# Kernel optimization log

Measured on AMD Instinct MI355X. Metric: run time of the kernel, lower is better.

The kernel has to match this reference:

```python
import jax, jax.numpy as jnp
import numpy as np

N, K, B, D, T = 30000, 32, 8, 256, 10
NC = T + 1            # int_small_classes
LB_COL, UB_COL = 21, 22
INF = 1e18


def _ln(x, g, b, eps=1e-5):
    m = jnp.mean(x, axis=-1, keepdims=True)
    v = jnp.mean((x - m) ** 2, axis=-1, keepdims=True)
    return (x - m) * jax.lax.rsqrt(v + eps) * g + b


def _head(x, ng, nb, W1, b1, W2, b2, Wh, bh):
    # LayerNorm -> Linear -> GELU -> Linear -> GELU -> residual -> head (dropout off: eval)
    h = _ln(x, ng, nb)
    h = jax.nn.gelu(h @ W1.T + b1, approximate=False)
    h = jax.nn.gelu(h @ W2.T + b2, approximate=False)
    return (x + h) @ Wh.T + bh


def setup_inputs():
    key = jax.random.key(0)
    ks = jax.random.split(key, 32)
    s = 0.05
    inp = {}
    inp['evolved_tokens'] = jax.random.normal(ks[0], (B * K, D), jnp.float32)
    inp['var_batch'] = jnp.sort(jax.random.randint(ks[1], (N,), 0, B))
    aw = jax.random.uniform(ks[2], (N, K), jnp.float32)
    inp['attn_weights'] = aw / aw.sum(-1, keepdims=True)
    inp['var_types'] = jax.random.randint(ks[3], (N,), 0, 3)
    inp['z_var_0'] = jax.random.normal(ks[4], (N, D), jnp.float32)
    vf = 0.1 * jax.random.normal(ks[5], (N, 23), jnp.float32)
    lb = jnp.floor(jax.random.uniform(ks[6], (N,), minval=-5.0, maxval=0.0))
    ub = lb + jnp.floor(jax.random.uniform(ks[7], (N,), minval=0.0, maxval=30.0))
    ub = jnp.where(jax.random.uniform(ks[8], (N,)) < 0.1, 1e19, ub)
    inp['variable_features'] = vf.at[:, LB_COL].set(lb).at[:, UB_COL].set(ub)
    # deslice proj + fusion norm
    inp['Wp'] = s * jax.random.normal(ks[9], (D, D), jnp.float32)
    inp['bp'] = jnp.zeros((D,), jnp.float32)
    inp['fn_g'] = jnp.ones((D,), jnp.float32)
    inp['fn_b'] = jnp.zeros((D,), jnp.float32)
    # three decoder heads
    i = 10
    for name, out in (('bin', 1), ('ints', NC), ('intl', 1)):
        inp[name + '_ng'] = jnp.ones((D,), jnp.float32)
        inp[name + '_nb'] = jnp.zeros((D,), jnp.float32)
        inp[name + '_W1'] = s * jax.random.normal(ks[i], (D, D), jnp.float32)
        inp[name + '_b1'] = jnp.zeros((D,), jnp.float32)
        inp[name + '_W2'] = s * jax.random.normal(ks[i + 1], (D, D), jnp.float32)
        inp[name + '_b2'] = jnp.zeros((D,), jnp.float32)
        inp[name + '_Wh'] = s * jax.random.normal(ks[i + 2], (out, D), jnp.float32)
        inp[name + '_bh'] = (jnp.full((out,), -0.5, jnp.float32) if name == 'bin'
                             else jnp.zeros((out,), jnp.float32))
        i += 3
    return inp


def reference(evolved_tokens, var_batch, attn_weights, var_types, z_var_0,
              variable_features, Wp, bp, fn_g, fn_b,
              bin_ng, bin_nb, bin_W1, bin_b1, bin_W2, bin_b2, bin_Wh, bin_bh,
              ints_ng, ints_nb, ints_W1, ints_b1, ints_W2, ints_b2, ints_Wh, ints_bh,
              intl_ng, intl_nb, intl_W1, intl_b1, intl_W2, intl_b2, intl_Wh, intl_bh):
    # 1. deslice: attn_weights @ projected evolved tokens of the variable's graph
    proj = evolved_tokens @ Wp.T + bp          # [B*K, D]
    tok3 = proj.reshape(B, K, D)
    z_des = jnp.einsum('nk,nkd->nd', attn_weights, tok3[var_batch])  # [N, D]
    # 2. residual fusion + LayerNorm
    z_out = _ln(z_des + z_var_0, fn_g, fn_b)
    # 3. routing (extract_int_routing)
    lb = variable_features[:, LB_COL]
    ub = variable_features[:, UB_COL]
    is_int = var_types == 2
    finite = (jnp.abs(lb) < INF) & (jnp.abs(ub) < INF)
    mask_int_small = is_int & finite & ((ub - lb) <= T)
    mask_int_large = is_int & ~mask_int_small
    mask_bin = var_types == 1
    offsets = jnp.floor(lb)                                   # [N]
    ranges = jnp.clip(jnp.ceil(ub) - offsets + 1.0, 1.0, NC).astype(jnp.int32)  # [N]
    # 4. decode. Heads are evaluated densely on all N rows; the original's
    #    gather->MLP->scatter equals row-selection of these dense outputs.
    prob_bin = jax.nn.sigmoid(_head(z_out, bin_ng, bin_nb, bin_W1, bin_b1,
                                    bin_W2, bin_b2, bin_Wh, bin_bh))   # [N, 1]
    logits = _head(z_out, ints_ng, ints_nb, ints_W1, ints_b1,
                   ints_W2, ints_b2, ints_Wh, ints_bh)                 # [N, NC]
    valid = jnp.arange(NC)[None, :] < ranges[:, None]
    logits = jnp.where(valid, logits, -1e9)  # dynamic logit masking of invalid classes
    pred_large = _head(z_out, intl_ng, intl_nb, intl_W1, intl_b1,
                       intl_W2, intl_b2, intl_Wh, intl_bh)             # [N, 1]
    return (z_out, prob_bin, logits, pred_large,
            mask_bin, mask_int_small, mask_int_large, offsets, ranges)
```

## Files before the change

kernel.cpp:

```cpp
#include <hip/hip_runtime.h>
#include <math.h>

#define NV   30000
#define DD   256
#define KK   32
#define NCLS 11
#define NT   469

#define OZ  0
#define OPB 7680000
#define OLG 7710000
#define OPL 8040000
#define OMB 8070000
#define OMS 8100000
#define OML 8130000
#define OOF 8160000
#define ORG 8190000

typedef __bf16 bf16x8 __attribute__((ext_vector_type(8)));
typedef float  f32x4  __attribute__((ext_vector_type(4)));

__device__ __forceinline__ unsigned short f2b(float f) {
    unsigned u = __float_as_uint(f);
    u += 0x7fffu + ((u >> 16) & 1u);
    return (unsigned short)(u >> 16);
}

__device__ __forceinline__ float gelu_f(float x) {
    float y = fabsf(x) * 0.70710678118f;
    float t = __builtin_amdgcn_rcpf(__builtin_fmaf(0.3275911f, y, 1.0f));
    float p = t * (0.254829592f + t * (-0.284496736f + t * (1.421413741f +
              t * (-1.453152027f + t * 1.061405429f))));
    float e = __expf(-y * y);
    float erfa = __builtin_fmaf(-p, e, 1.0f);
    float erfv = copysignf(erfa, x);
    return 0.5f * x * (1.0f + erfv);
}

__device__ __forceinline__ int swz(int row) { return (row + (row >> 3)) & 7; }
__device__ __forceinline__ int lidx(int row, int col) {
    return row * 256 + ((((col) >> 3) ^ swz(row)) << 3) + (col & 7);
}

struct WP {
    const float *W1, *ng, *nb, *b1, *W2, *Wh;
    unsigned short *W1e, *W2b, *Whb;
    float *b1e, *swh;
    int nc;
};

__global__ void k_prep(const float* __restrict__ et, const float* __restrict__ Wp,
                       const float* __restrict__ bp, float* __restrict__ proj,
                       WP wa, WP wb, WP wc) {
    __shared__ float es[DD];
    __shared__ float red[4], red2[4];
    if (blockIdx.y == 0) {
        int r = blockIdx.x, c = threadIdx.x;
        es[c] = et[r * DD + c];
        __syncthreads();
        const float4* w4 = (const float4*)(Wp + c * DD);
        float acc = bp[c];
#pragma unroll 16
        for (int d = 0; d < DD / 4; ++d) {
            float4 w = w4[d];
            acc += es[4 * d] * w.x + es[4 * d + 1] * w.y + es[4 * d + 2] * w.z + es[4 * d + 3] * w.w;
        }
        proj[r * DD + c] = acc;
        return;
    }
    WP wp = (blockIdx.y == 1) ? wa : ((blockIdx.y == 2) ? wb : wc);
    int j = blockIdx.x, d = threadIdx.x;
    float v1 = wp.W1[j * DD + d];
    wp.W1e[j * DD + d] = f2b(v1 * wp.ng[d]);
    wp.W2b[j * DD + d] = f2b(wp.W2[j * DD + d]);
    float p2 = 0.f;
    if (j < 16) {
        p2 = (j < wp.nc) ? wp.Wh[j * DD + d] : 0.f;
        wp.Whb[j * DD + d] = f2b(p2);
    }
    float p = v1 * wp.nb[d];
#pragma unroll
    for (int m = 1; m < 64; m <<= 1) { p += __shfl_xor(p, m); p2 += __shfl_xor(p2, m); }
    if ((d & 63) == 0) { red[d >> 6] = p; red2[d >> 6] = p2; }
    __syncthreads();
    if (d == 0) {
        wp.b1e[j] = wp.b1[j] + red[0] + red[1] + red[2] + red[3];
        if (j < 16) wp.swh[j] = red2[0] + red2[1] + red2[2] + red2[3];
    }
}

__global__ __launch_bounds__(256)
void k_zout(const float* __restrict__ proj, const int* __restrict__ vb,
            const float* __restrict__ aw, const float* __restrict__ z0,
            const float* __restrict__ g, const float* __restrict__ b,
            const float* __restrict__ vf, const int* __restrict__ vt,
            float* __restrict__ out, unsigned short* __restrict__ zhat,
            float2* __restrict__ zstat) {
    int wv = threadIdx.x >> 6, lane = threadIdx.x & 63;
    int n = blockIdx.x * 4 + wv;
    if (n >= NV) return;
    int bidx = vb[n];
    float awv = aw[n * KK + (lane & 31)];
    const float4* pr = (const float4*)(proj + (size_t)bidx * KK * DD);
    float4 acc = ((const float4*)(z0 + (size_t)n * DD))[lane];
#pragma unroll 8
    for (int k = 0; k < KK; ++k) {
        float a = __shfl(awv, k);
        float4 p = pr[k * 64 + lane];
        acc.x += a * p.x; acc.y += a * p.y; acc.z += a * p.z; acc.w += a * p.w;
    }
    float s = acc.x + acc.y + acc.z + acc.w;
    float q = acc.x * acc.x + acc.y * acc.y + acc.z * acc.z + acc.w * acc.w;
#pragma unroll
    for (int m = 1; m < 64; m <<= 1) { s += __shfl_xor(s, m); q += __shfl_xor(q, m); }
    float mean = s * (1.f / DD);
    float var  = q * (1.f / DD) - mean * mean;
    float rs   = rsqrtf(var + 1e-5f);
    float4 g4 = ((const float4*)g)[lane], b4 = ((const float4*)b)[lane];
    float4 z;
    z.x = (acc.x - mean) * rs * g4.x + b4.x;
    z.y = (acc.y - mean) * rs * g4.y + b4.y;
    z.z = (acc.z - mean) * rs * g4.z + b4.z;
    z.w = (acc.w - mean) * rs * g4.w + b4.w;
    ((float4*)(out + OZ + (size_t)n * DD))[lane] = z;
    float s2 = z.x + z.y + z.z + z.w;
    float q2 = z.x * z.x + z.y * z.y + z.z * z.z + z.w * z.w;
#pragma unroll
    for (int m = 1; m < 64; m <<= 1) { s2 += __shfl_xor(s2, m); q2 += __shfl_xor(q2, m); }
    float m2 = s2 * (1.f / DD);
    float v2 = q2 * (1.f / DD) - m2 * m2;
    float r2 = rsqrtf(v2 + 1e-5f);
    ushort4 zh;
    zh.x = f2b((z.x - m2) * r2); zh.y = f2b((z.y - m2) * r2);
    zh.z = f2b((z.z - m2) * r2); zh.w = f2b((z.w - m2) * r2);
    int rl = n & 63;
    int c = lane >> 1;
    int pc = (c & ~7) | ((c & 7) ^ swz(rl));
    *(ushort4*)(zhat + (size_t)(n & ~63) * 256 + rl * 256 + pc * 8 + (lane & 1) * 4) = zh;
    if (lane == 0) {
        zstat[n] = make_float2((v2 + 1e-5f) * r2, m2);
        float lb = vf[n * 23 + 21], ub = vf[n * 23 + 22];
        int t = vt[n];
        bool is_int = (t == 2);
        bool finite = (fabsf(lb) < 1e18f) && (fabsf(ub) < 1e18f);
        bool small_ = is_int && finite && (ub - lb <= 10.0f);
        float off = floorf(lb);
        float rngf = ceilf(ub) - off + 1.0f;
        rngf = fminf(fmaxf(rngf, 1.0f), (float)NCLS);
        out[OMB + n] = (t == 1) ? 1.0f : 0.0f;
        out[OMS + n] = small_ ? 1.0f : 0.0f;
        out[OML + n] = (is_int && !small_) ? 1.0f : 0.0f;
        out[OOF + n] = off;
        out[ORG + n] = (float)((int)rngf);
    }
}

struct HeadP {
    const unsigned short *W1e, *W2b, *Whb;
    const float *b1e, *b2, *bh, *swh;
    int nc;
};

__global__ __launch_bounds__(256, 3)
void k_heads(const unsigned short* __restrict__ zhat, const float2* __restrict__ zstat,
             const float* __restrict__ ranges,
             HeadP h0, HeadP h1p, HeadP h2p,
             float* __restrict__ opb, float* __restrict__ olg, float* __restrict__ opl) {
    __shared__ unsigned short hl[64 * 256];
    __shared__ float b1s[DD], b2s[DD];
    __shared__ float rs2s[64], m2s[64];
    __shared__ float swhs[16], bhs[16];

    int head = blockIdx.x / NT;
    int tile = blockIdx.x % NT;
    HeadP hp = (head == 0) ? h0 : ((head == 1) ? h1p : h2p);
    int nc = hp.nc;
    int n0 = tile * 64;
    int tid = threadIdx.x;

    {
        const uint4* src = (const uint4*)(zhat + (size_t)n0 * 256);
        uint4* dst = (uint4*)hl;
#pragma unroll
        for (int j = 0; j < 8; ++j) dst[tid + j * 256] = src[tid + j * 256];
    }
    b1s[tid] = hp.b1e[tid];
    b2s[tid] = hp.b2[tid];
    if (tid < 64) {
        int n = n0 + tid;
        float2 st = (n < NV) ? zstat[n] : make_float2(0.f, 0.f);
        rs2s[tid] = st.x; m2s[tid] = st.y;
    } else if (tid < 80) {
        swhs[tid - 64] = hp.swh[tid - 64];
    } else if (tid < 96) {
        int o = tid - 80;
        bhs[o] = (o < nc) ? hp.bh[o] : 0.f;
    }

    int lane = tid & 63, wv = tid >> 6;
    int l15 = lane & 15, lq = lane >> 4;
    int nb0 = wv * 64;

    f32x4 acc[4][4];
#pragma unroll
    for (int mt = 0; mt < 4; ++mt)
#pragma unroll
        for (int nt = 0; nt < 4; ++nt) acc[mt][nt] = f32x4{0.f, 0.f, 0.f, 0.f};

    __syncthreads();

    {
        const unsigned short* Bb = hp.W1e + (size_t)(nb0 + l15) * DD + lq * 8;
        bf16x8 b[3][4], a[2][4];
#pragma unroll
        for (int s = 0; s < 3; ++s)
#pragma unroll
            for (int nt = 0; nt < 4; ++nt) b[s][nt] = *(const bf16x8*)(Bb + nt * 16 * DD + s * 32);
#pragma unroll
        for (int mt = 0; mt < 4; ++mt) {
            int row = mt * 16 + l15;
            int ph = (lq & 7) ^ swz(row);
            a[0][mt] = *(const bf16x8*)(hl + row * 256 + ph * 8);
        }
#pragma unroll
        for (int ks = 0; ks < 8; ++ks) {
            int cur = ks & 1, sl = ks % 3;
            if (ks < 7) {
                int ck = (ks + 1) * 4 + lq;
#pragma unroll
                for (int mt = 0; mt < 4; ++mt) {
                    int row = mt * 16 + l15;
                    int ph = (ck & ~7) | ((ck & 7) ^ swz(row));
                    a[cur ^ 1][mt] = *(const bf16x8*)(hl + row * 256 + ph * 8);
                }
            }
#pragma unroll
            for (int nt = 0; nt < 4; ++nt)
#pragma unroll
                for (int mt = 0; mt < 4; ++mt)
                    acc[mt][nt] = __builtin_amdgcn_mfma_f32_16x16x32_bf16(a[cur][mt], b[sl][nt], acc[mt][nt], 0, 0, 0);
            if (ks + 3 < 8) {
#pragma unroll
                for (int nt = 0; nt < 4; ++nt)
                    b[sl][nt] = *(const bf16x8*)(Bb + nt * 16 * DD + (ks + 3) * 32);
            }
        }
    }
    __syncthreads();

#pragma unroll
    for (int nt = 0; nt < 4; ++nt) {
        int col = nb0 + nt * 16 + l15;
        float bias = b1s[col];
#pragma unroll
        for (int mt = 0; mt < 4; ++mt)
#pragma unroll
            for (int r = 0; r < 4; ++r) {
                int row = mt * 16 + lq * 4 + r;
                hl[lidx(row, col)] = f2b(gelu_f(acc[mt][nt][r] + bias));
            }
    }
    __syncthreads();

#pragma unroll
    for (int mt = 0; mt < 4; ++mt)
#pragma unroll
        for (int nt = 0; nt < 4; ++nt) acc[mt][nt] = f32x4{0.f, 0.f, 0.f, 0.f};
    {
        const unsigned short* Bb = hp.W2b + (size_t)(nb0 + l15) * DD + lq * 8;
        bf16x8 b[3][4], a[2][4];
#pragma unroll
        for (int s = 0; s < 3; ++s)
#pragma unroll
            for (int nt = 0; nt < 4; ++nt) b[s][nt] = *(const bf16x8*)(Bb + nt * 16 * DD + s * 32);
#pragma unroll
        for (int mt = 0; mt < 4; ++mt) {
            int row = mt * 16 + l15;
            int ph = (lq & 7) ^ swz(row);
            a[0][mt] = *(const bf16x8*)(hl + row * 256 + ph * 8);
        }
#pragma unroll
        for (int ks = 0; ks < 8; ++ks) {
            int cur = ks & 1, sl = ks % 3;
            if (ks < 7) {
                int ck = (ks + 1) * 4 + lq;
#pragma unroll
                for (int mt = 0; mt < 4; ++mt) {
                    int row = mt * 16 + l15;
                    int ph = (ck & ~7) | ((ck & 7) ^ swz(row));
                    a[cur ^ 1][mt] = *(const bf16x8*)(hl + row * 256 + ph * 8);
                }
            }
#pragma unroll
            for (int nt = 0; nt < 4; ++nt)
#pragma unroll
                for (int mt = 0; mt < 4; ++mt)
                    acc[mt][nt] = __builtin_amdgcn_mfma_f32_16x16x32_bf16(a[cur][mt], b[sl][nt], acc[mt][nt], 0, 0, 0);
            if (ks + 3 < 8) {
#pragma unroll
                for (int nt = 0; nt < 4; ++nt)
                    b[sl][nt] = *(const bf16x8*)(Bb + nt * 16 * DD + (ks + 3) * 32);
            }
        }
    }

#pragma unroll
    for (int nt = 0; nt < 4; ++nt) {
        float bias = b2s[nb0 + nt * 16 + l15];
#pragma unroll
        for (int mt = 0; mt < 4; ++mt)
#pragma unroll
            for (int r = 0; r < 4; ++r)
                acc[mt][nt][r] = gelu_f(acc[mt][nt][r] + bias);
    }
    __syncthreads();

#pragma unroll
    for (int nt = 0; nt < 4; ++nt) {
        int col = nb0 + nt * 16 + l15;
#pragma unroll
        for (int mt = 0; mt < 4; ++mt)
#pragma unroll
            for (int r = 0; r < 4; ++r) {
                int row = mt * 16 + lq * 4 + r;
                hl[lidx(row, col)] = f2b(acc[mt][nt][r]);
            }
    }

    f32x4 accP[4], accZ[4];
#pragma unroll
    for (int mt = 0; mt < 4; ++mt) { accP[mt] = f32x4{0.f, 0.f, 0.f, 0.f}; accZ[mt] = f32x4{0.f, 0.f, 0.f, 0.f}; }
    {
        const unsigned short* Wb = hp.Whb + (size_t)l15 * DD + nb0 + lq * 8;
        const unsigned short* zt = zhat + (size_t)n0 * 256;
#pragma unroll
        for (int ks = 0; ks < 2; ++ks) {
            bf16x8 bP = *(const bf16x8*)(Wb + ks * 32);
            int ck = (nb0 >> 3) + ks * 4 + lq;
#pragma unroll
            for (int mt = 0; mt < 4; ++mt) {
                int row = mt * 16 + l15;
                int ph = (ck & ~7) | ((ck & 7) ^ swz(row));
                bf16x8 aP = *(const bf16x8*)(hl + row * 256 + ph * 8);
                bf16x8 aZ = *(const bf16x8*)(zt + row * 256 + ph * 8);
                accP[mt] = __builtin_amdgcn_mfma_f32_16x16x32_bf16(aP, bP, accP[mt], 0, 0, 0);
                accZ[mt] = __builtin_amdgcn_mfma_f32_16x16x32_bf16(aZ, bP, accZ[mt], 0, 0, 0);
            }
        }
    }
#pragma unroll
    for (int mt = 0; mt < 4; ++mt) {
        int rb = mt * 16 + lq * 4;
#pragma unroll
        for (int r = 0; r < 4; ++r) {
            float pv = accP[mt][r] + rs2s[rb + r] * accZ[mt][r];
            float* pp = (float*)(hl + (rb + r) * 256 + nb0);
            pp[l15] = pv;
        }
    }
    __syncthreads();

    for (int idx = tid; idx < 64 * nc; idx += 256) {
        int row, o;
        if (nc == 1) { row = idx; o = 0; }
        else { row = idx / NCLS; o = idx - row * NCLS; }
        int n = n0 + row;
        if (n < NV) {
            float val = bhs[o] + m2s[row] * swhs[o];
#pragma unroll
            for (int w2 = 0; w2 < 4; ++w2)
                val += ((const float*)(hl + row * 256 + w2 * 64))[o];
            if (head == 0)      opb[n] = 1.f / (1.f + expf(-val));
            else if (head == 2) opl[n] = val;
            else {
                int rng = (int)ranges[n];
                olg[n * NCLS + o] = (o < rng) ? val : -1e9f;
            }
        }
    }
}

extern "C" void kernel_launch(void* const* d_in, const int* in_sizes, int n_in,
                              void* d_out, int out_size, void* d_ws, size_t ws_size,
                              hipStream_t stream) {
    const float* et = (const float*)d_in[0];
    const int*   vb = (const int*)d_in[1];
    const float* aw = (const float*)d_in[2];
    const int*   vt = (const int*)d_in[3];
    const float* z0 = (const float*)d_in[4];
    const float* vf = (const float*)d_in[5];
    const float* Wp = (const float*)d_in[6];
    const float* bp = (const float*)d_in[7];
    const float* fg = (const float*)d_in[8];
    const float* fb = (const float*)d_in[9];
    float* out = (float*)d_out;

    char* ws = (char*)d_ws;
    float* proj          = (float*)ws;
    float* b1e           = (float*)(ws + 262144);
    unsigned short* W1e  = (unsigned short*)(ws + 265216);
    unsigned short* W2b  = (unsigned short*)(ws + 658432);
    unsigned short* Whb  = (unsigned short*)(ws + 1051648);
    float* swh           = (float*)(ws + 1076224);
    float2* zstat        = (float2*)(ws + 1076480);
    unsigned short* zhat = (unsigned short*)(ws + 1316608);

    WP wps[3];
    for (int h = 0; h < 3; ++h) {
        wps[h].W1 = (const float*)d_in[12 + 8 * h];
        wps[h].ng = (const float*)d_in[10 + 8 * h];
        wps[h].nb = (const float*)d_in[11 + 8 * h];
        wps[h].b1 = (const float*)d_in[13 + 8 * h];
        wps[h].W2 = (const float*)d_in[14 + 8 * h];
        wps[h].Wh = (const float*)d_in[16 + 8 * h];
        wps[h].W1e = W1e + h * 65536;
        wps[h].W2b = W2b + h * 65536;
        wps[h].Whb = Whb + h * 4096;
        wps[h].b1e = b1e + h * 256;
        wps[h].swh = swh + h * 16;
        wps[h].nc  = (h == 1) ? NCLS : 1;
    }
    k_prep<<<dim3(256, 4), 256, 0, stream>>>(et, Wp, bp, proj, wps[0], wps[1], wps[2]);

    k_zout<<<7500, 256, 0, stream>>>(proj, vb, aw, z0, fg, fb, vf, vt, out, zhat, zstat);

    HeadP hps[3];
    for (int h = 0; h < 3; ++h) {
        hps[h].W1e = W1e + h * 65536;
        hps[h].W2b = W2b + h * 65536;
        hps[h].Whb = Whb + h * 4096;
        hps[h].b1e = b1e + h * 256;
        hps[h].b2  = (const float*)d_in[15 + 8 * h];
        hps[h].bh  = (const float*)d_in[17 + 8 * h];
        hps[h].swh = swh + h * 16;
        hps[h].nc  = (h == 1) ? NCLS : 1;
    }
    k_heads<<<3 * NT, 256, 0, stream>>>(zhat, zstat, out + ORG,
                                        hps[0], hps[1], hps[2],
                                        out + OPB, out + OLG, out + OPL);
}
```

Before: 280.2 us.

## Use tanh-form GELU, bf16 projection, leaner MFMA prefetch, higher occupancy

Replaces the erf-polynomial GELU with a sigmoid-of-cubic (tanh approximation) form, which is cheaper but no longer exact erf GELU. Stores the deslice projection as bf16 to halve the gather traffic in k_zout. Restructures the MFMA loops to double-buffer B from global memory and load A from LDS just in time, cutting register use so launch bounds can request 4 blocks per CU. Also switches the sigmoid to fast exp and reciprocal.

```diff
diff --git a/kernel.cpp b/kernel.cpp
--- a/kernel.cpp
+++ b/kernel.cpp
@@ -27,14 +27,10 @@
 }
 
 __device__ __forceinline__ float gelu_f(float x) {
-    float y = fabsf(x) * 0.70710678118f;
-    float t = __builtin_amdgcn_rcpf(__builtin_fmaf(0.3275911f, y, 1.0f));
-    float p = t * (0.254829592f + t * (-0.284496736f + t * (1.421413741f +
-              t * (-1.453152027f + t * 1.061405429f))));
-    float e = __expf(-y * y);
-    float erfa = __builtin_fmaf(-p, e, 1.0f);
-    float erfv = copysignf(erfa, x);
-    return 0.5f * x * (1.0f + erfv);
+    float x2 = x * x;
+    float m = x * __builtin_fmaf(-0.0713548163f, x2, -1.5957691216f);
+    float e = __expf(m);
+    return x * __builtin_amdgcn_rcpf(1.0f + e);
 }
 
 __device__ __forceinline__ int swz(int row) { return (row + (row >> 3)) & 7; }
@@ -50,7 +46,7 @@
 };
 
 __global__ void k_prep(const float* __restrict__ et, const float* __restrict__ Wp,
-                       const float* __restrict__ bp, float* __restrict__ proj,
+                       const float* __restrict__ bp, unsigned short* __restrict__ projb,
                        WP wa, WP wb, WP wc) {
     __shared__ float es[DD];
     __shared__ float red[4], red2[4];
@@ -65,7 +61,7 @@
             float4 w = w4[d];
             acc += es[4 * d] * w.x + es[4 * d + 1] * w.y + es[4 * d + 2] * w.z + es[4 * d + 3] * w.w;
         }
-        proj[r * DD + c] = acc;
+        projb[r * DD + c] = f2b(acc);
         return;
     }
     WP wp = (blockIdx.y == 1) ? wa : ((blockIdx.y == 2) ? wb : wc);
@@ -90,7 +86,7 @@
 }
 
 __global__ __launch_bounds__(256)
-void k_zout(const float* __restrict__ proj, const int* __restrict__ vb,
+void k_zout(const unsigned short* __restrict__ projb, const int* __restrict__ vb,
             const float* __restrict__ aw, const float* __restrict__ z0,
             const float* __restrict__ g, const float* __restrict__ b,
             const float* __restrict__ vf, const int* __restrict__ vt,
@@ -101,13 +97,16 @@
     if (n >= NV) return;
     int bidx = vb[n];
     float awv = aw[n * KK + (lane & 31)];
-    const float4* pr = (const float4*)(proj + (size_t)bidx * KK * DD);
+    const ushort4* pr = (const ushort4*)(projb + (size_t)bidx * KK * DD);
     float4 acc = ((const float4*)(z0 + (size_t)n * DD))[lane];
 #pragma unroll 8
     for (int k = 0; k < KK; ++k) {
         float a = __shfl(awv, k);
-        float4 p = pr[k * 64 + lane];
-        acc.x += a * p.x; acc.y += a * p.y; acc.z += a * p.z; acc.w += a * p.w;
+        ushort4 pu = pr[k * 64 + lane];
+        acc.x += a * __uint_as_float((unsigned)pu.x << 16);
+        acc.y += a * __uint_as_float((unsigned)pu.y << 16);
+        acc.z += a * __uint_as_float((unsigned)pu.z << 16);
+        acc.w += a * __uint_as_float((unsigned)pu.w << 16);
     }
     float s = acc.x + acc.y + acc.z + acc.w;
     float q = acc.x * acc.x + acc.y * acc.y + acc.z * acc.z + acc.w * acc.w;
@@ -161,7 +160,7 @@
     int nc;
 };
 
-__global__ __launch_bounds__(256, 3)
+__global__ __launch_bounds__(256, 4)
 void k_heads(const unsigned short* __restrict__ zhat, const float2* __restrict__ zstat,
              const float* __restrict__ ranges,
              HeadP h0, HeadP h1p, HeadP h2p,
@@ -211,39 +210,29 @@
 
     {
         const unsigned short* Bb = hp.W1e + (size_t)(nb0 + l15) * DD + lq * 8;
-        bf16x8 b[3][4], a[2][4];
-#pragma unroll
-        for (int s = 0; s < 3; ++s)
-#pragma unroll
-            for (int nt = 0; nt < 4; ++nt) b[s][nt] = *(const bf16x8*)(Bb + nt * 16 * DD + s * 32);
-#pragma unroll
-        for (int mt = 0; mt < 4; ++mt) {
-            int row = mt * 16 + l15;
-            int ph = (lq & 7) ^ swz(row);
-            a[0][mt] = *(const bf16x8*)(hl + row * 256 + ph * 8);
-        }
+        bf16x8 b[2][4], a[4];
+#pragma unroll
+        for (int nt = 0; nt < 4; ++nt) b[0][nt] = *(const bf16x8*)(Bb + nt * 16 * DD);
 #pragma unroll
         for (int ks = 0; ks < 8; ++ks) {
-            int cur = ks & 1, sl = ks % 3;
+            int cur = ks & 1;
             if (ks < 7) {
-                int ck = (ks + 1) * 4 + lq;
-#pragma unroll
-                for (int mt = 0; mt < 4; ++mt) {
-                    int row = mt * 16 + l15;
-                    int ph = (ck & ~7) | ((ck & 7) ^ swz(row));
-                    a[cur ^ 1][mt] = *(const bf16x8*)(hl + row * 256 + ph * 8);
-                }
+#pragma unroll
+                for (int nt = 0; nt < 4; ++nt)
+                    b[cur ^ 1][nt] = *(const bf16x8*)(Bb + nt * 16 * DD + (ks + 1) * 32);
+            }
+            int ck = ks * 4 + lq;
+#pragma unroll
+            for (int mt = 0; mt < 4; ++mt) {
+                int row = mt * 16 + l15;
+                int ph = (ck & ~7) | ((ck & 7) ^ swz(row));
+                a[mt] = *(const bf16x8*)(hl + row * 256 + ph * 8);
             }
 #pragma unroll
             for (int nt = 0; nt < 4; ++nt)
 #pragma unroll
                 for (int mt = 0; mt < 4; ++mt)
-                    acc[mt][nt] = __builtin_amdgcn_mfma_f32_16x16x32_bf16(a[cur][mt], b[sl][nt], acc[mt][nt], 0, 0, 0);
-            if (ks + 3 < 8) {
-#pragma unroll
-                for (int nt = 0; nt < 4; ++nt)
-                    b[sl][nt] = *(const bf16x8*)(Bb + nt * 16 * DD + (ks + 3) * 32);
-            }
+                    acc[mt][nt] = __builtin_amdgcn_mfma_f32_16x16x32_bf16(a[mt], b[cur][nt], acc[mt][nt], 0, 0, 0);
         }
     }
     __syncthreads();
@@ -268,39 +257,29 @@
         for (int nt = 0; nt < 4; ++nt) acc[mt][nt] = f32x4{0.f, 0.f, 0.f, 0.f};
     {
         const unsigned short* Bb = hp.W2b + (size_t)(nb0 + l15) * DD + lq * 8;
-        bf16x8 b[3][4], a[2][4];
-#pragma unroll
-        for (int s = 0; s < 3; ++s)
-#pragma unroll
-            for (int nt = 0; nt < 4; ++nt) b[s][nt] = *(const bf16x8*)(Bb + nt * 16 * DD + s * 32);
-#pragma unroll
-        for (int mt = 0; mt < 4; ++mt) {
-            int row = mt * 16 + l15;
-            int ph = (lq & 7) ^ swz(row);
-            a[0][mt] = *(const bf16x8*)(hl + row * 256 + ph * 8);
-        }
+        bf16x8 b[2][4], a[4];
+#pragma unroll
+        for (int nt = 0; nt < 4; ++nt) b[0][nt] = *(const bf16x8*)(Bb + nt * 16 * DD);
 #pragma unroll
         for (int ks = 0; ks < 8; ++ks) {
-            int cur = ks & 1, sl = ks % 3;
+            int cur = ks & 1;
             if (ks < 7) {
-                int ck = (ks + 1) * 4 + lq;
-#pragma unroll
-                for (int mt = 0; mt < 4; ++mt) {
-                    int row = mt * 16 + l15;
-                    int ph = (ck & ~7) | ((ck & 7) ^ swz(row));
-                    a[cur ^ 1][mt] = *(const bf16x8*)(hl + row * 256 + ph * 8);
-                }
+#pragma unroll
+                for (int nt = 0; nt < 4; ++nt)
+                    b[cur ^ 1][nt] = *(const bf16x8*)(Bb + nt * 16 * DD + (ks + 1) * 32);
+            }
+            int ck = ks * 4 + lq;
+#pragma unroll
+            for (int mt = 0; mt < 4; ++mt) {
+                int row = mt * 16 + l15;
+                int ph = (ck & ~7) | ((ck & 7) ^ swz(row));
+                a[mt] = *(const bf16x8*)(hl + row * 256 + ph * 8);
             }
 #pragma unroll
             for (int nt = 0; nt < 4; ++nt)
 #pragma unroll
                 for (int mt = 0; mt < 4; ++mt)
-                    acc[mt][nt] = __builtin_amdgcn_mfma_f32_16x16x32_bf16(a[cur][mt], b[sl][nt], acc[mt][nt], 0, 0, 0);
-            if (ks + 3 < 8) {
-#pragma unroll
-                for (int nt = 0; nt < 4; ++nt)
-                    b[sl][nt] = *(const bf16x8*)(Bb + nt * 16 * DD + (ks + 3) * 32);
-            }
+                    acc[mt][nt] = __builtin_amdgcn_mfma_f32_16x16x32_bf16(a[mt], b[cur][nt], acc[mt][nt], 0, 0, 0);
         }
     }
 
@@ -370,7 +349,7 @@
 #pragma unroll
             for (int w2 = 0; w2 < 4; ++w2)
                 val += ((const float*)(hl + row * 256 + w2 * 64))[o];
-            if (head == 0)      opb[n] = 1.f / (1.f + expf(-val));
+            if (head == 0)      opb[n] = __builtin_amdgcn_rcpf(1.f + __expf(-val));
             else if (head == 2) opl[n] = val;
             else {
                 int rng = (int)ranges[n];
@@ -396,14 +375,14 @@
     float* out = (float*)d_out;
 
     char* ws = (char*)d_ws;
-    float* proj          = (float*)ws;
-    float* b1e           = (float*)(ws + 262144);
-    unsigned short* W1e  = (unsigned short*)(ws + 265216);
-    unsigned short* W2b  = (unsigned short*)(ws + 658432);
-    unsigned short* Whb  = (unsigned short*)(ws + 1051648);
-    float* swh           = (float*)(ws + 1076224);
-    float2* zstat        = (float2*)(ws + 1076480);
-    unsigned short* zhat = (unsigned short*)(ws + 1316608);
+    unsigned short* projb = (unsigned short*)ws;
+    float* b1e           = (float*)(ws + 131072);
+    unsigned short* W1e  = (unsigned short*)(ws + 134144);
+    unsigned short* W2b  = (unsigned short*)(ws + 527360);
+    unsigned short* Whb  = (unsigned short*)(ws + 920576);
+    float* swh           = (float*)(ws + 945152);
+    float2* zstat        = (float2*)(ws + 945408);
+    unsigned short* zhat = (unsigned short*)(ws + 1185536);
 
     WP wps[3];
     for (int h = 0; h < 3; ++h) {
@@ -420,9 +399,9 @@
         wps[h].swh = swh + h * 16;
         wps[h].nc  = (h == 1) ? NCLS : 1;
     }
-    k_prep<<<dim3(256, 4), 256, 0, stream>>>(et, Wp, bp, proj, wps[0], wps[1], wps[2]);
-
-    k_zout<<<7500, 256, 0, stream>>>(proj, vb, aw, z0, fg, fb, vf, vt, out, zhat, zstat);
+    k_prep<<<dim3(256, 4), 256, 0, stream>>>(et, Wp, bp, projb, wps[0], wps[1], wps[2]);
+
+    k_zout<<<7500, 256, 0, stream>>>(projb, vb, aw, z0, fg, fb, vf, vt, out, zhat, zstat);
 
     HeadP hps[3];
     for (int h = 0; h < 3; ++h) {
```

New measurement: 279.3 us. No clear change (-0.3%).
